# Kernel tuning notes

Measured on AMD Instinct MI355X. Metric: run time of the kernel, lower is better.

Reference implementation:

```python
import jax, jax.numpy as jnp
import numpy as np

B, S, D = 4, 4096, 1024          # batch, seq, in/out features
H = 128                          # controller_hidden_dim
K = 8                            # num_spectral_bases
R = 8                            # low_rank_rank
OR = 8                           # orthogonal_rank
RES_SCALE = 1.0; SPEC_SCALE = 1.0; LR_SCALE = 1.0; ROT_SCALE = 1.0
LN_EPS = 1e-5


def setup_inputs() -> dict:
    key = jax.random.key(0)
    ks = jax.random.split(key, 16)
    g = lambda k, shape, scale=0.02: jax.random.normal(k, shape, jnp.float32) * scale
    return dict(
        x=jax.random.normal(ks[0], (B, S, D), jnp.float32),
        # base linear (teacher-aligned base)
        W_base=g(ks[1], (D, D)), b_base=jnp.zeros((D,), jnp.float32),
        # pooled-token conditioner: LayerNorm -> Linear -> GELU -> Linear
        ln_g=jnp.ones((D,), jnp.float32), ln_b=jnp.zeros((D,), jnp.float32),
        Wc1=g(ks[2], (D, H)), bc1=jnp.zeros((H,), jnp.float32),
        Wc2=g(ks[3], (H, H)), bc2=jnp.zeros((H,), jnp.float32),
        # gate heads
        W_rot_gate=g(ks[4], (H, 1)), b_rot_gate=jnp.zeros((1,), jnp.float32),
        W_rot_coeff=g(ks[5], (H, OR)), b_rot_coeff=jnp.zeros((OR,), jnp.float32),
        W_spec_gate=g(ks[6], (H, K)), b_spec_gate=jnp.zeros((K,), jnp.float32),
        W_lr_coeff=g(ks[7], (H, R)), b_lr_coeff=jnp.zeros((R,), jnp.float32),
        # spectral basis operator: input basis U, output basis V
        U_spec=g(ks[8], (K, D), 0.05), V_spec=g(ks[9], (K, D), 0.05),
        # low-rank residual operator
        U_lr=g(ks[10], (R, D), 0.05), V_lr=g(ks[11], (R, D), 0.05),
        # low-rank orthogonal mixer generators (skew-symmetric pairs)
        A_orth=g(ks[12], (OR, D), 0.05), B_orth=g(ks[13], (OR, D), 0.05),
    )


def reference(x, W_base, b_base, ln_g, ln_b, Wc1, bc1, Wc2, bc2,
              W_rot_gate, b_rot_gate, W_rot_coeff, b_rot_coeff,
              W_spec_gate, b_spec_gate, W_lr_coeff, b_lr_coeff,
              U_spec, V_spec, U_lr, V_lr, A_orth, B_orth):
    # --- pooled token conditioner: mean pool -> LN -> MLP -> hidden h [B,H]
    pooled = x.mean(axis=1)                                   # [B, D]
    mu = pooled.mean(-1, keepdims=True)
    var = pooled.var(-1, keepdims=True)
    z = (pooled - mu) * jax.lax.rsqrt(var + LN_EPS) * ln_g + ln_b
    h = jax.nn.gelu(z @ Wc1 + bc1) @ Wc2 + bc2                # [B, H]

    # --- conditioner-produced gates
    rot_gate = jax.nn.sigmoid(h @ W_rot_gate + b_rot_gate)    # [B, 1]
    rot_coeff = jnp.tanh(h @ W_rot_coeff + b_rot_coeff)       # [B, OR]
    spec_gate = jnp.tanh(h @ W_spec_gate + b_spec_gate)       # [B, K]
    lr_coeff = jnp.tanh(h @ W_lr_coeff + b_lr_coeff)          # [B, R]

    # --- low-rank orthogonal mixer: x_rot = x + gate * x @ G^T,
    #     G = sum_k c_k (a_k b_k^T - b_k a_k^T) (skew-symmetric generator)
    pa = jnp.einsum('bsi,ki->bsk', x, A_orth)
    pb = jnp.einsum('bsi,ki->bsk', x, B_orth)
    rot = (jnp.einsum('bsk,bk,ki->bsi', pb, rot_coeff, A_orth)
           - jnp.einsum('bsk,bk,ki->bsi', pa, rot_coeff, B_orth))
    x_rot = x + (ROT_SCALE * rot_gate)[:, None, :] * rot      # [B,S,D]

    # --- spectral basis operator: gated rank-K map through fixed bases
    s = jnp.einsum('bsi,ki->bsk', x_rot, U_spec)
    y_spec = SPEC_SCALE * jnp.einsum('bsk,bk,ko->bso', s, spec_gate, V_spec)

    # --- low-rank residual operator
    t = jnp.einsum('bsi,ki->bsk', x_rot, U_lr)
    y_lr = LR_SCALE * jnp.einsum('bsk,bk,ko->bso', t, lr_coeff, V_lr)

    # --- teacher-aligned base + gated residual operators
    return x_rot @ W_base + b_base + RES_SCALE * (y_spec + y_lr)
```

## Files before the change

### kernel.cpp

```cpp
#include <hip/hip_runtime.h>

typedef unsigned short u16;
typedef unsigned int   u32;
typedef __bf16 bf16x8 __attribute__((ext_vector_type(8)));
typedef float  f32x4  __attribute__((ext_vector_type(4)));

#define DD 1024

__device__ __forceinline__ u16 f2bf(float f) {
  u32 u = __float_as_uint(f);
  u32 r = (u + 0x7FFFu + ((u >> 16) & 1u)) >> 16;
  return (u16)r;
}

typedef const __attribute__((address_space(1))) void* gp1;
typedef __attribute__((address_space(3))) void* lp3;
__device__ __forceinline__ void gll16(const void* g, void* l) {
  __builtin_amdgcn_global_load_lds((gp1)g, (lp3)l, 16, 0, 0);
}

template <bool XB>
__global__ __launch_bounds__(256) void k01_pre(
    const float* __restrict__ x, u16* __restrict__ xb, float* __restrict__ pooled,
    const float* __restrict__ W,
    const float* __restrict__ Ao, const float* __restrict__ Bo,
    const float* __restrict__ Us, const float* __restrict__ Ul,
    float* __restrict__ AWBW, float* __restrict__ Mbuf,
    u16* __restrict__ Pb, u16* __restrict__ Wt) {
  const int tid = threadIdx.x;
  int bid = blockIdx.x;
  if (bid < 256) {
    const int b = bid >> 6;
    const long r0 = (long)bid * 64;
    const int c0 = tid * 4;
    float s0 = 0.f, s1 = 0.f, s2 = 0.f, s3 = 0.f;
    for (int r = 0; r < 64; r++) {
      float4 v = *(const float4*)(x + (r0 + r) * DD + c0);
      if (XB) {
        ushort4 o;
        o.x = f2bf(v.x); o.y = f2bf(v.y); o.z = f2bf(v.z); o.w = f2bf(v.w);
        *(ushort4*)(xb + (r0 + r) * DD + c0) = o;
      }
      s0 += v.x; s1 += v.y; s2 += v.z; s3 += v.w;
    }
    atomicAdd(&pooled[b * DD + c0 + 0], s0);
    atomicAdd(&pooled[b * DD + c0 + 1], s1);
    atomicAdd(&pooled[b * DD + c0 + 2], s2);
    atomicAdd(&pooled[b * DD + c0 + 3], s3);
    return;
  }
  bid -= 256;
  if (bid < 32) {
    __shared__ float red2[2][128][16];
    const int m = bid;
    const int n = (m & 7) * 128 + (tid & 127), q = m >> 3, ih = tid >> 7;
    float acc[16];
#pragma unroll
    for (int k = 0; k < 16; k++) acc[k] = 0.f;
    const int ib = q * 256 + ih * 128;
    for (int i = ib; i < ib + 128; i++) {
      float wv = W[(long)i * DD + n];
#pragma unroll
      for (int k = 0; k < 8; k++) {
        acc[k]     += Ao[k * DD + i] * wv;
        acc[k + 8] += Bo[k * DD + i] * wv;
      }
    }
#pragma unroll
    for (int k = 0; k < 16; k++) red2[ih][tid & 127][k] = acc[k];
    __syncthreads();
    if (ih == 0)
#pragma unroll
      for (int k = 0; k < 16; k++)
        atomicAdd(&AWBW[k * DD + n], red2[0][tid][k] + red2[1][tid][k]);
  } else if (bid < 36) {
    __shared__ float red[64][4];
    const int m = bid - 32;
    const float* L  = (m == 0 || m == 2) ? Ao : Bo;
    const float* Rr = (m < 2) ? Us : Ul;
    const int o = tid >> 2, ch = tid & 3;
    const int k = o >> 3, kp = o & 7;
    float a = 0.f;
    for (int i = ch * 256; i < ch * 256 + 256; i++)
      a += L[(long)k * DD + i] * Rr[(long)kp * DD + i];
    red[o][ch] = a;
    __syncthreads();
    if (tid < 64) Mbuf[m * 64 + tid] = red[tid][0] + red[tid][1] + red[tid][2] + red[tid][3];
  } else if (bid < 40) {
    const int m = bid - 36;
    const float* src = m == 0 ? Ao : m == 1 ? Bo : m == 2 ? Us : Ul;
#pragma unroll
    for (int j = 0; j < 8; j++)
      for (int q = 0; q < 4; q++) {
        int i = q * 256 + tid;
        Pb[(m * 8 + j) * DD + i] = f2bf(src[j * DD + i]);
      }
  } else {
    __shared__ u16 T[64][66];
    const int t = bid - 40, tr = t >> 4, tc = t & 15;
#pragma unroll
    for (int q2 = 0; q2 < 16; q2++) {
      int idx = q2 * 256 + tid, r = idx >> 6, c = idx & 63;
      T[r][c] = f2bf(W[(long)(tr * 64 + r) * DD + tc * 64 + c]);
    }
    __syncthreads();
#pragma unroll
    for (int q2 = 0; q2 < 16; q2++) {
      int idx = q2 * 256 + tid, c = idx >> 6, r = idx & 63;
      Wt[(long)(tc * 64 + c) * DD + tr * 64 + r] = T[r][c];
    }
  }
}

__global__ __launch_bounds__(256) void k2ab(
    const float* __restrict__ pooledsum,
    const float* __restrict__ lng, const float* __restrict__ lnb,
    const float* __restrict__ Wc1, float* __restrict__ h1pre,
    const float* __restrict__ AWBW, const float* Vs, const float* Vl,
    const float* bc1, const float* Wc2, const float* bc2,
    const float* Wrg, const float* brg, const float* Wrc, const float* brc,
    const float* Wsg, const float* bsg, const float* Wlc, const float* blc,
    float* __restrict__ gates, u16* __restrict__ RwT,
    u32* __restrict__ cnt) {
  const int tid = threadIdx.x;
  if (blockIdx.x < 32) {
    __shared__ float zs[1024];
    __shared__ float wsh[16384];
    __shared__ float red[256];
    const int b = blockIdx.x >> 3, ch = blockIdx.x & 7;
    float4 v = *(const float4*)(pooledsum + b * DD + tid * 4);
    v.x *= (1.f / 4096.f); v.y *= (1.f / 4096.f); v.z *= (1.f / 4096.f); v.w *= (1.f / 4096.f);
    float s = v.x + v.y + v.z + v.w;
    float sq = v.x * v.x + v.y * v.y + v.z * v.z + v.w * v.w;
    red[tid] = s; __syncthreads();
    for (int st = 128; st > 0; st >>= 1) { if (tid < st) red[tid] += red[tid + st]; __syncthreads(); }
    float mu = red[0] * (1.f / 1024.f);
    __syncthreads();
    red[tid] = sq; __syncthreads();
    for (int st = 128; st > 0; st >>= 1) { if (tid < st) red[tid] += red[tid + st]; __syncthreads(); }
    float var = red[0] * (1.f / 1024.f) - mu * mu;
    float rs = rsqrtf(var + 1e-5f);
    __syncthreads();
    {
      float4 g = *(const float4*)(lng + tid * 4);
      float4 be = *(const float4*)(lnb + tid * 4);
      zs[tid * 4 + 0] = (v.x - mu) * rs * g.x + be.x;
      zs[tid * 4 + 1] = (v.y - mu) * rs * g.y + be.y;
      zs[tid * 4 + 2] = (v.z - mu) * rs * g.z + be.z;
      zs[tid * 4 + 3] = (v.w - mu) * rs * g.w + be.w;
    }
    {
      const float4* src = (const float4*)(Wc1 + ch * 16384);
      float4* dst = (float4*)wsh;
#pragma unroll
      for (int it = 0; it < 16; it++) dst[it * 256 + tid] = src[it * 256 + tid];
    }
    __syncthreads();
    const int j = tid & 127, half = tid >> 7;
    float a = 0.f;
#pragma unroll 8
    for (int dd = 0; dd < 64; dd++) {
      int ldi = half * 64 + dd;
      a += zs[ch * 128 + ldi] * wsh[ldi * 128 + j];
    }
    red[tid] = a;
    __syncthreads();
    if (tid < 128) atomicAdd(&h1pre[b * 128 + tid], red[tid] + red[tid + 128]);
    __syncthreads();
    if (tid == 0) atomicAdd(cnt, 1u);
  } else if (blockIdx.x < 36) {
    __shared__ float wc2sh[16384];
    __shared__ float h1s[128], hb[128];
    __shared__ float red[256];
    __shared__ float hw[3200];
    const int b = (int)blockIdx.x - 32;
    {
      const float4* src = (const float4*)Wc2;
      float4* dst = (float4*)wc2sh;
#pragma unroll
      for (int it = 0; it < 16; it++) dst[it * 256 + tid] = src[it * 256 + tid];
    }
    for (int idx = tid; idx < 3200; idx += 256) {
      float vv;
      if (idx < 128)       vv = Wrg[idx];
      else if (idx < 1152) vv = Wrc[idx - 128];
      else if (idx < 2176) vv = Wsg[idx - 1152];
      else                 vv = Wlc[idx - 2176];
      hw[idx] = vv;
    }
    if (tid == 0) {
      while (atomicAdd(cnt, 0u) < 32u) __builtin_amdgcn_s_sleep(8);
    }
    __syncthreads();
    if (tid < 128) {
      float hv = atomicAdd(&h1pre[b * 128 + tid], 0.f) + bc1[tid];
      float th = tanhf(0.7978845608028654f * (hv + 0.044715f * hv * hv * hv));
      h1s[tid] = 0.5f * hv * (1.f + th);
    }
    __syncthreads();
    const int i = tid & 127, half = tid >> 7;
    float a = 0.f;
#pragma unroll 8
    for (int k = 0; k < 64; k++) {
      int kk = half * 64 + k;
      a += h1s[kk] * wc2sh[kk * 128 + i];
    }
    red[tid] = a;
    __syncthreads();
    if (tid < 128) hb[tid] = red[tid] + red[tid + 128] + bc2[tid];
    __syncthreads();
    if (tid < 25) {
      float acc;
      if (tid == 0) {
        acc = brg[0];
        for (int k = 0; k < 128; k++) acc += hb[k] * hw[k];
        red[0] = 1.f / (1.f + expf(-acc));
      } else if (tid < 9) {
        int ci = tid - 1; acc = brc[ci];
        for (int k = 0; k < 128; k++) acc += hb[k] * hw[128 + k * 8 + ci];
        red[tid] = tanhf(acc);
      } else if (tid < 17) {
        int ci = tid - 9; acc = bsg[ci];
        for (int k = 0; k < 128; k++) acc += hb[k] * hw[1152 + k * 8 + ci];
        red[tid] = tanhf(acc);
      } else {
        int ci = tid - 17; acc = blc[ci];
        for (int k = 0; k < 128; k++) acc += hb[k] * hw[2176 + k * 8 + ci];
        red[tid] = tanhf(acc);
      }
    }
    __syncthreads();
    if (tid < 24) {
      float g = red[0];
      gates[b * 32 + tid] = (tid < 8) ? g * red[1 + tid] : red[1 + tid];
    }
  } else {
    const int n = (int)(blockIdx.x - 36) * 256 + tid;
#pragma unroll
    for (int j = 0; j < 8; j++) {
      RwT[n * 32 + j]      = f2bf(AWBW[j * DD + n]);
      RwT[n * 32 + 8 + j]  = f2bf(AWBW[(8 + j) * DD + n]);
      RwT[n * 32 + 16 + j] = f2bf(Vs[(long)j * DD + n]);
      RwT[n * 32 + 24 + j] = f2bf(Vl[(long)j * DD + n]);
    }
  }
}

__global__ __launch_bounds__(256, 3) void k3a_fused(
    const u16* __restrict__ xb, const u16* __restrict__ Wt,
    const u16* __restrict__ Pb, const float* __restrict__ gates,
    const float* __restrict__ Mbuf, const u16* __restrict__ RwT,
    const float* __restrict__ bb, float* __restrict__ out) {
  __shared__ __align__(16) char smem[38912];
  const int tid = threadIdx.x, lane = tid & 63, w = tid >> 6;
  const int quad = lane >> 4, lrow = lane & 15;
  const int bidx = blockIdx.x;
  const int bm = (bidx & 7) * 16 + (bidx >> 6);
  const int bn = (bidx >> 3) & 7;
  const long m0 = (long)bm * 128;
  const int n0 = bn * 128;
  const int batch = bm >> 5;
  float* Ml = (float*)(smem + 36864);
  float* gl = (float*)(smem + 37888);
  Ml[tid] = Mbuf[tid];
  if (tid < 24) gl[tid] = gates[batch * 32 + tid];
  const int mw = (w & 1) * 64, nw = (w >> 1) * 64;
  const int sr = lane >> 2, sc = (lane & 3) * 16;
  const char* xbp = (const char*)xb;
  const char* wtp = (const char*)Wt;
  const char* pbp = (const char*)Pb;
  const long aOff0 = (m0 + (long)w * 16 + sr) * 2048 + sc;
  const long aOff1 = aOff0 + 4 * 16 * 2048;
  const long bOff0 = ((long)n0 + w * 16 + sr) * 2048 + sc;
  const long bOff1 = bOff0 + 4 * 16 * 2048;
  const long pOff  = ((long)w * 16 + sr) * 2048 + sc;
  const int d0 = w * 1024 + lane * 16;

  f32x4 acc[4][4] = {};
  f32x4 acc2[2][2] = {};

  gll16(xbp + aOff0, smem + d0);
  gll16(xbp + aOff1, smem + d0 + 4096);
  gll16(wtp + bOff0, smem + 16384 + d0);
  gll16(wtp + bOff1, smem + 16384 + d0 + 4096);
  if (w < 2) gll16(pbp + pOff, smem + 32768 + d0);
  __syncthreads();

  int cur = 0;
  for (int kc = 0; kc < 32; kc++) {
    if (kc < 31) {
      const long ko = (long)(kc + 1) * 64;
      const int s = cur ^ 1;
      gll16(xbp + aOff0 + ko, smem + s * 8192 + d0);
      gll16(xbp + aOff1 + ko, smem + s * 8192 + d0 + 4096);
      gll16(wtp + bOff0 + ko, smem + 16384 + s * 8192 + d0);
      gll16(wtp + bOff1 + ko, smem + 16384 + s * 8192 + d0 + 4096);
      if (w < 2) gll16(pbp + pOff + ko, smem + 32768 + s * 2048 + d0);
    }
    const u16* At = (const u16*)(smem + cur * 8192);
    const u16* Bt = (const u16*)(smem + 16384 + cur * 8192);
    const u16* Pt = (const u16*)(smem + 32768 + cur * 2048);
    bf16x8 af[4], bq[4], af2[2], bp[2];
#pragma unroll
    for (int tm = 0; tm < 4; tm++)
      af[tm] = *(const bf16x8*)(At + (mw + tm * 16 + lrow) * 32 + quad * 8);
#pragma unroll
    for (int tn = 0; tn < 4; tn++)
      bq[tn] = *(const bf16x8*)(Bt + (nw + tn * 16 + lrow) * 32 + quad * 8);
#pragma unroll
    for (int t2 = 0; t2 < 2; t2++)
      af2[t2] = *(const bf16x8*)(At + (w * 32 + t2 * 16 + lrow) * 32 + quad * 8);
#pragma unroll
    for (int tn2 = 0; tn2 < 2; tn2++)
      bp[tn2] = *(const bf16x8*)(Pt + (tn2 * 16 + lrow) * 32 + quad * 8);
#pragma unroll
    for (int tm = 0; tm < 4; tm++)
#pragma unroll
      for (int tn = 0; tn < 4; tn++)
        acc[tm][tn] = __builtin_amdgcn_mfma_f32_16x16x32_bf16(af[tm], bq[tn], acc[tm][tn], 0, 0, 0);
#pragma unroll
    for (int t2 = 0; t2 < 2; t2++)
#pragma unroll
      for (int tn2 = 0; tn2 < 2; tn2++)
        acc2[t2][tn2] = __builtin_amdgcn_mfma_f32_16x16x32_bf16(af2[t2], bp[tn2], acc2[t2][tn2], 0, 0, 0);
    __syncthreads();
    cur ^= 1;
  }

  {
    const char* rwp = (const char*)RwT;
    const long rOff = ((long)n0 + w * 16 + sr) * 64 + sc;
    gll16(rwp + rOff, smem + 16384 + d0);
    gll16(rwp + rOff + 64 * 64, smem + 16384 + d0 + 4096);
  }
  float* projF = (float*)smem;
#pragma unroll
  for (int t2 = 0; t2 < 2; t2++)
#pragma unroll
    for (int tn2 = 0; tn2 < 2; tn2++)
#pragma unroll
      for (int r = 0; r < 4; r++)
        projF[(w * 32 + t2 * 16 + quad * 4 + r) * 32 + tn2 * 16 + lrow] = acc2[t2][tn2][r];
  __syncthreads();
  if (tid < 128) {
    float pr[32];
#pragma unroll
    for (int j = 0; j < 32; j++) pr[j] = projF[tid * 32 + j];
    float wo[32];
#pragma unroll
    for (int k = 0; k < 8; k++) { wo[k] = gl[k] * pr[8 + k]; wo[8 + k] = -gl[k] * pr[k]; }
#pragma unroll
    for (int kp = 0; kp < 8; kp++) {
      float sv = pr[16 + kp], tv = pr[24 + kp];
#pragma unroll
      for (int k = 0; k < 8; k++) {
        float gpb = gl[k] * pr[8 + k], gpa = gl[k] * pr[k];
        sv += gpb * Ml[k * 8 + kp]       - gpa * Ml[64 + k * 8 + kp];
        tv += gpb * Ml[128 + k * 8 + kp] - gpa * Ml[192 + k * 8 + kp];
      }
      wo[16 + kp] = gl[8 + kp] * sv;
      wo[24 + kp] = gl[16 + kp] * tv;
    }
    u16* wLds = (u16*)(smem + 24576);
#pragma unroll
    for (int j = 0; j < 32; j++) wLds[tid * 32 + j] = f2bf(wo[j]);
  }
  __syncthreads();
  {
    const u16* wL = (const u16*)(smem + 24576);
    const u16* Rt = (const u16*)(smem + 16384);
    bf16x8 af[4], bq[4];
#pragma unroll
    for (int tm = 0; tm < 4; tm++)
      af[tm] = *(const bf16x8*)(wL + (mw + tm * 16 + lrow) * 32 + quad * 8);
#pragma unroll
    for (int tn = 0; tn < 4; tn++)
      bq[tn] = *(const bf16x8*)(Rt + (nw + tn * 16 + lrow) * 32 + quad * 8);
#pragma unroll
    for (int tm = 0; tm < 4; tm++)
#pragma unroll
      for (int tn = 0; tn < 4; tn++)
        acc[tm][tn] = __builtin_amdgcn_mfma_f32_16x16x32_bf16(af[tm], bq[tn], acc[tm][tn], 0, 0, 0);
  }
#pragma unroll
  for (int tn = 0; tn < 4; tn++) {
    const int col = n0 + nw + tn * 16 + lrow;
    const float bias = bb[col];
#pragma unroll
    for (int tm = 0; tm < 4; tm++)
#pragma unroll
      for (int r = 0; r < 4; r++) {
        long row = m0 + mw + tm * 16 + quad * 4 + r;
        out[row * DD + col] = acc[tm][tn][r] + bias;
      }
  }
}

template <bool XB>
__global__ __launch_bounds__(256) void k3_fused(
    const float* __restrict__ xf, const u16* __restrict__ xb,
    const u16* __restrict__ Wt, const u16* __restrict__ Pb,
    const float* __restrict__ gates, const float* __restrict__ Mbuf,
    const u16* __restrict__ RwT, const float* __restrict__ bb,
    float* __restrict__ out) {
  __shared__ __align__(16) u16 At[4096];
  __shared__ __align__(16) u16 Bt[4096];
  __shared__ __align__(16) u16 Pt[1024];
  __shared__ float projF[128 * 32];
  __shared__ __align__(16) u16 wLds[4096];
  __shared__ float Ml[256];
  __shared__ float gl[24];
  const int tid = threadIdx.x, lane = tid & 63, w = tid >> 6;
  const int quad = lane >> 4, lrow = lane & 15;
  const int bn = blockIdx.x & 7, bm = blockIdx.x >> 3;
  const long m0 = (long)bm * 128;
  const int n0 = bn * 128;
  const int batch = bm >> 5;
  Ml[tid] = Mbuf[tid];
  if (tid < 24) gl[tid] = gates[batch * 32 + tid];
  const int mw = (w & 1) * 64, nw = (w >> 1) * 64;
  const int p0 = (w * 2) * 1024 + lane * 16, p1 = p0 + 1024;
  f32x4 acc[4][4] = {};
  f32x4 acc2[2][2] = {};
  for (int kc = 0; kc < 32; kc++) {
    uint4 vb0 = *(const uint4*)((const char*)Wt + (long)(n0 + (p0 >> 6)) * 2048 + kc * 64 + (p0 & 63));
    uint4 vb1 = *(const uint4*)((const char*)Wt + (long)(n0 + (p1 >> 6)) * 2048 + kc * 64 + (p1 & 63));
    uint4 vp;
    if (tid < 128)
      vp = *(const uint4*)((const char*)Pb + (tid >> 2) * 2048 + kc * 64 + (tid & 3) * 16);
    if (XB) {
      uint4 va0 = *(const uint4*)((const char*)xb + (m0 + (p0 >> 6)) * 2048 + kc * 64 + (p0 & 63));
      uint4 va1 = *(const uint4*)((const char*)xb + (m0 + (p1 >> 6)) * 2048 + kc * 64 + (p1 & 63));
      *(uint4*)((char*)At + p0) = va0;
      *(uint4*)((char*)At + p1) = va1;
    } else {
      ushort4 oa[4];
#pragma unroll
      for (int i = 0; i < 4; i++) {
        int fi = i * 256 + tid, row = fi >> 3, c4 = (fi & 7) * 4;
        float4 v = *(const float4*)(xf + (m0 + row) * DD + kc * 32 + c4);
        oa[i].x = f2bf(v.x); oa[i].y = f2bf(v.y); oa[i].z = f2bf(v.z); oa[i].w = f2bf(v.w);
      }
#pragma unroll
      for (int i = 0; i < 4; i++) {
        int fi = i * 256 + tid, row = fi >> 3, c4 = (fi & 7) * 4;
        *(ushort4*)(At + row * 32 + c4) = oa[i];
      }
    }
    *(uint4*)((char*)Bt + p0) = vb0;
    *(uint4*)((char*)Bt + p1) = vb1;
    if (tid < 128) *(uint4*)((char*)Pt + (tid >> 2) * 64 + (tid & 3) * 16) = vp;
    __syncthreads();
    bf16x8 af[4], bq[4], af2[2], bp[2];
#pragma unroll
    for (int tm = 0; tm < 4; tm++)
      af[tm] = *(const bf16x8*)(At + (mw + tm * 16 + lrow) * 32 + quad * 8);
#pragma unroll
    for (int tn = 0; tn < 4; tn++)
      bq[tn] = *(const bf16x8*)(Bt + (nw + tn * 16 + lrow) * 32 + quad * 8);
#pragma unroll
    for (int t2 = 0; t2 < 2; t2++)
      af2[t2] = *(const bf16x8*)(At + (w * 32 + t2 * 16 + lrow) * 32 + quad * 8);
#pragma unroll
    for (int tn2 = 0; tn2 < 2; tn2++)
      bp[tn2] = *(const bf16x8*)(Pt + (tn2 * 16 + lrow) * 32 + quad * 8);
#pragma unroll
    for (int tm = 0; tm < 4; tm++)
#pragma unroll
      for (int tn = 0; tn < 4; tn++)
        acc[tm][tn] = __builtin_amdgcn_mfma_f32_16x16x32_bf16(af[tm], bq[tn], acc[tm][tn], 0, 0, 0);
#pragma unroll
    for (int t2 = 0; t2 < 2; t2++)
#pragma unroll
      for (int tn2 = 0; tn2 < 2; tn2++)
        acc2[t2][tn2] = __builtin_amdgcn_mfma_f32_16x16x32_bf16(af2[t2], bp[tn2], acc2[t2][tn2], 0, 0, 0);
    __syncthreads();
  }
#pragma unroll
  for (int t2 = 0; t2 < 2; t2++)
#pragma unroll
    for (int tn2 = 0; tn2 < 2; tn2++)
#pragma unroll
      for (int r = 0; r < 4; r++)
        projF[(w * 32 + t2 * 16 + quad * 4 + r) * 32 + tn2 * 16 + lrow] = acc2[t2][tn2][r];
  {
    uint4 vr0 = *(const uint4*)((const char*)RwT + (long)(n0 + (p0 >> 6)) * 64 + (p0 & 63));
    uint4 vr1 = *(const uint4*)((const char*)RwT + (long)(n0 + (p1 >> 6)) * 64 + (p1 & 63));
    *(uint4*)((char*)Bt + p0) = vr0;
    *(uint4*)((char*)Bt + p1) = vr1;
  }
  __syncthreads();
  if (tid < 128) {
    float pr[32];
#pragma unroll
    for (int j = 0; j < 32; j++) pr[j] = projF[tid * 32 + j];
    float wo[32];
#pragma unroll
    for (int k = 0; k < 8; k++) { wo[k] = gl[k] * pr[8 + k]; wo[8 + k] = -gl[k] * pr[k]; }
#pragma unroll
    for (int kp = 0; kp < 8; kp++) {
      float sv = pr[16 + kp], tv = pr[24 + kp];
#pragma unroll
      for (int k = 0; k < 8; k++) {
        float gpb = gl[k] * pr[8 + k], gpa = gl[k] * pr[k];
        sv += gpb * Ml[k * 8 + kp]       - gpa * Ml[64 + k * 8 + kp];
        tv += gpb * Ml[128 + k * 8 + kp] - gpa * Ml[192 + k * 8 + kp];
      }
      wo[16 + kp] = gl[8 + kp] * sv;
      wo[24 + kp] = gl[16 + kp] * tv;
    }
#pragma unroll
    for (int j = 0; j < 32; j++) wLds[tid * 32 + j] = f2bf(wo[j]);
  }
  __syncthreads();
  {
    bf16x8 af[4], bq[4];
#pragma unroll
    for (int tm = 0; tm < 4; tm++)
      af[tm] = *(const bf16x8*)(wLds + (mw + tm * 16 + lrow) * 32 + quad * 8);
#pragma unroll
    for (int tn = 0; tn < 4; tn++)
      bq[tn] = *(const bf16x8*)(Bt + (nw + tn * 16 + lrow) * 32 + quad * 8);
#pragma unroll
    for (int tm = 0; tm < 4; tm++)
#pragma unroll
      for (int tn = 0; tn < 4; tn++)
        acc[tm][tn] = __builtin_amdgcn_mfma_f32_16x16x32_bf16(af[tm], bq[tn], acc[tm][tn], 0, 0, 0);
  }
#pragma unroll
  for (int tn = 0; tn < 4; tn++) {
    const int col = n0 + nw + tn * 16 + lrow;
    const float bias = bb[col];
#pragma unroll
    for (int tm = 0; tm < 4; tm++)
#pragma unroll
      for (int r = 0; r < 4; r++) {
        long row = m0 + mw + tm * 16 + quad * 4 + r;
        out[row * DD + col] = acc[tm][tn][r] + bias;
      }
  }
}

extern "C" void kernel_launch(void* const* d_in, const int* in_sizes, int n_in,
                              void* d_out, int out_size, void* d_ws, size_t ws_size,
                              hipStream_t stream) {
  const float* x   = (const float*)d_in[0];
  const float* Wb  = (const float*)d_in[1];
  const float* bb  = (const float*)d_in[2];
  const float* lng = (const float*)d_in[3];
  const float* lnb = (const float*)d_in[4];
  const float* Wc1 = (const float*)d_in[5];
  const float* bc1 = (const float*)d_in[6];
  const float* Wc2 = (const float*)d_in[7];
  const float* bc2 = (const float*)d_in[8];
  const float* Wrg = (const float*)d_in[9];
  const float* brg = (const float*)d_in[10];
  const float* Wrc = (const float*)d_in[11];
  const float* brc = (const float*)d_in[12];
  const float* Wsg = (const float*)d_in[13];
  const float* bsg = (const float*)d_in[14];
  const float* Wlc = (const float*)d_in[15];
  const float* blc = (const float*)d_in[16];
  const float* Us  = (const float*)d_in[17];
  const float* Vs  = (const float*)d_in[18];
  const float* Ul  = (const float*)d_in[19];
  const float* Vl  = (const float*)d_in[20];
  const float* Ao  = (const float*)d_in[21];
  const float* Bo  = (const float*)d_in[22];

  char* ws = (char*)d_ws;
  float* pooled = (float*)(ws + 0);
  float* AWBW   = (float*)(ws + 16384);
  float* h1pre  = (float*)(ws + 81920);
  float* gates  = (float*)(ws + 83968);
  float* Mbuf   = (float*)(ws + 84480);
  u32*   cnt    = (u32*)  (ws + 85504);
  u16*   RwT    = (u16*)  (ws + 85568);
  u16*   Pb     = (u16*)  (ws + 151104);
  u16*   Wt     = (u16*)  (ws + 216640);
  u16*   xb     = (u16*)  (ws + 2313792);
  float* out    = (float*)d_out;

  const bool modeA = ws_size >= (size_t)2313792 + 33554432;

  (void)hipMemsetAsync(d_ws, 0, 85568, stream);
  if (modeA)
    k01_pre<true><<<552, 256, 0, stream>>>(x, xb, pooled, Wb, Ao, Bo, Us, Ul,
                                           AWBW, Mbuf, Pb, Wt);
  else
    k01_pre<false><<<552, 256, 0, stream>>>(x, xb, pooled, Wb, Ao, Bo, Us, Ul,
                                            AWBW, Mbuf, Pb, Wt);
  k2ab<<<40, 256, 0, stream>>>(pooled, lng, lnb, Wc1, h1pre,
                               AWBW, Vs, Vl, bc1, Wc2, bc2,
                               Wrg, brg, Wrc, brc, Wsg, bsg, Wlc, blc,
                               gates, RwT, cnt);
  if (modeA)
    k3a_fused<<<1024, 256, 0, stream>>>(xb, Wt, Pb, gates, Mbuf, RwT, bb, out);
  else
    k3_fused<false><<<1024, 256, 0, stream>>>(x, xb, Wt, Pb, gates, Mbuf, RwT, bb, out);
}
```

Before: 298.7 us.

## Split pooling into more XCD-mapped blocks and reuse A fragments for projection MFMA

The pooling/bf16-conversion stage now launches 1024 blocks of 16 rows each instead of 256 blocks of 64, with row blocks mapped so consecutive rows stay on the same XCD. This adds parallelism to a memory-bound pass at the cost of four times as many atomics. In the fused GEMM, the side projection MFMAs reuse the main A fragments already loaded (each wave covers its 64 rows by a 16-column slice of P), removing the extra LDS reads of af2. The projF staging store is XOR-swizzled to avoid bank conflicts.

```diff
diff --git a/kernel.cpp b/kernel.cpp
--- a/kernel.cpp
+++ b/kernel.cpp
@@ -29,12 +29,14 @@
     u16* __restrict__ Pb, u16* __restrict__ Wt) {
   const int tid = threadIdx.x;
   int bid = blockIdx.x;
-  if (bid < 256) {
-    const int b = bid >> 6;
-    const long r0 = (long)bid * 64;
+  if (bid < 1024) {
+    const int xcd = bid & 7, local = bid >> 3;
+    const int rb = xcd * 128 + local;
+    const int b = rb >> 8;
+    const long r0 = (long)rb * 16;
     const int c0 = tid * 4;
     float s0 = 0.f, s1 = 0.f, s2 = 0.f, s3 = 0.f;
-    for (int r = 0; r < 64; r++) {
+    for (int r = 0; r < 16; r++) {
       float4 v = *(const float4*)(x + (r0 + r) * DD + c0);
       if (XB) {
         ushort4 o;
@@ -49,7 +51,7 @@
     atomicAdd(&pooled[b * DD + c0 + 3], s3);
     return;
   }
-  bid -= 256;
+  bid -= 1024;
   if (bid < 32) {
     __shared__ float red2[2][128][16];
     const int m = bid;
@@ -265,6 +267,7 @@
   Ml[tid] = Mbuf[tid];
   if (tid < 24) gl[tid] = gates[batch * 32 + tid];
   const int mw = (w & 1) * 64, nw = (w >> 1) * 64;
+  const int pc0 = (w >> 1) * 16;
   const int sr = lane >> 2, sc = (lane & 3) * 16;
   const char* xbp = (const char*)xb;
   const char* wtp = (const char*)Wt;
@@ -277,7 +280,7 @@
   const int d0 = w * 1024 + lane * 16;
 
   f32x4 acc[4][4] = {};
-  f32x4 acc2[2][2] = {};
+  f32x4 acc2[4] = {};
 
   gll16(xbp + aOff0, smem + d0);
   gll16(xbp + aOff1, smem + d0 + 4096);
@@ -300,29 +303,22 @@
     const u16* At = (const u16*)(smem + cur * 8192);
     const u16* Bt = (const u16*)(smem + 16384 + cur * 8192);
     const u16* Pt = (const u16*)(smem + 32768 + cur * 2048);
-    bf16x8 af[4], bq[4], af2[2], bp[2];
+    bf16x8 af[4], bq[4], bp;
 #pragma unroll
     for (int tm = 0; tm < 4; tm++)
       af[tm] = *(const bf16x8*)(At + (mw + tm * 16 + lrow) * 32 + quad * 8);
 #pragma unroll
     for (int tn = 0; tn < 4; tn++)
       bq[tn] = *(const bf16x8*)(Bt + (nw + tn * 16 + lrow) * 32 + quad * 8);
-#pragma unroll
-    for (int t2 = 0; t2 < 2; t2++)
-      af2[t2] = *(const bf16x8*)(At + (w * 32 + t2 * 16 + lrow) * 32 + quad * 8);
-#pragma unroll
-    for (int tn2 = 0; tn2 < 2; tn2++)
-      bp[tn2] = *(const bf16x8*)(Pt + (tn2 * 16 + lrow) * 32 + quad * 8);
+    bp = *(const bf16x8*)(Pt + (pc0 + lrow) * 32 + quad * 8);
 #pragma unroll
     for (int tm = 0; tm < 4; tm++)
 #pragma unroll
       for (int tn = 0; tn < 4; tn++)
         acc[tm][tn] = __builtin_amdgcn_mfma_f32_16x16x32_bf16(af[tm], bq[tn], acc[tm][tn], 0, 0, 0);
 #pragma unroll
-    for (int t2 = 0; t2 < 2; t2++)
-#pragma unroll
-      for (int tn2 = 0; tn2 < 2; tn2++)
-        acc2[t2][tn2] = __builtin_amdgcn_mfma_f32_16x16x32_bf16(af2[t2], bp[tn2], acc2[t2][tn2], 0, 0, 0);
+    for (int tm = 0; tm < 4; tm++)
+      acc2[tm] = __builtin_amdgcn_mfma_f32_16x16x32_bf16(af[tm], bp, acc2[tm], 0, 0, 0);
     __syncthreads();
     cur ^= 1;
   }
@@ -335,17 +331,18 @@
   }
   float* projF = (float*)smem;
 #pragma unroll
-  for (int t2 = 0; t2 < 2; t2++)
-#pragma unroll
-    for (int tn2 = 0; tn2 < 2; tn2++)
-#pragma unroll
-      for (int r = 0; r < 4; r++)
-        projF[(w * 32 + t2 * 16 + quad * 4 + r) * 32 + tn2 * 16 + lrow] = acc2[t2][tn2][r];
+  for (int tm = 0; tm < 4; tm++)
+#pragma unroll
+    for (int r = 0; r < 4; r++) {
+      int row = mw + tm * 16 + quad * 4 + r;
+      int col = pc0 + lrow;
+      projF[row * 32 + (col ^ (row & 31))] = acc2[tm][r];
+    }
   __syncthreads();
   if (tid < 128) {
     float pr[32];
 #pragma unroll
-    for (int j = 0; j < 32; j++) pr[j] = projF[tid * 32 + j];
+    for (int j = 0; j < 32; j++) pr[j] = projF[tid * 32 + (j ^ (tid & 31))];
     float wo[32];
 #pragma unroll
     for (int k = 0; k < 8; k++) { wo[k] = gl[k] * pr[8 + k]; wo[8 + k] = -gl[k] * pr[k]; }
@@ -585,11 +582,11 @@
 
   (void)hipMemsetAsync(d_ws, 0, 85568, stream);
   if (modeA)
-    k01_pre<true><<<552, 256, 0, stream>>>(x, xb, pooled, Wb, Ao, Bo, Us, Ul,
-                                           AWBW, Mbuf, Pb, Wt);
+    k01_pre<true><<<1320, 256, 0, stream>>>(x, xb, pooled, Wb, Ao, Bo, Us, Ul,
+                                            AWBW, Mbuf, Pb, Wt);
   else
-    k01_pre<false><<<552, 256, 0, stream>>>(x, xb, pooled, Wb, Ao, Bo, Us, Ul,
-                                            AWBW, Mbuf, Pb, Wt);
+    k01_pre<false><<<1320, 256, 0, stream>>>(x, xb, pooled, Wb, Ao, Bo, Us, Ul,
+                                             AWBW, Mbuf, Pb, Wt);
   k2ab<<<40, 256, 0, stream>>>(pooled, lng, lnb, Wc1, h1pre,
                                AWBW, Vs, Vl, bc1, Wc2, bc2,
                                Wrg, brg, Wrc, brc, Wsg, bsg, Wlc, blc,
```

Result: slower. 320.5 us (+7.3%).
